# Optimization experiments

Hardware: AMD Instinct MI355X
Metric: run time of the kernel (lower is better)

The kernel has to match this reference:

```python
import jax, jax.numpy as jnp
import numpy as np

NEG_INF = -1e9  # matches torch masked_fill value


def setup_inputs() -> dict:
    key = jax.random.key(0)
    k1, k2, k3, k4, k5 = jax.random.split(key, 5)
    B, H, T, D = 2, 16, 2048, 64
    q = jax.random.normal(k1, (B, H, T, D), dtype=jnp.float32)
    k = jax.random.normal(k2, (B, H, T, D), dtype=jnp.float32)
    v = jax.random.normal(k3, (B, H, T, D), dtype=jnp.float32)
    mask = jax.random.randint(k4, (B, 1, 1, T), 0, 2, dtype=jnp.int32)
    relative_position_bias = jax.random.normal(k5, (1, H, T, T), dtype=jnp.float32)
    return {"q": q, "k": k, "v": v, "mask": mask,
            "relative_position_bias": relative_position_bias}


def reference(q, k, v, mask, relative_position_bias):
    head_dim = q.shape[-1]
    scale = 1.0 / jnp.sqrt(jnp.float32(head_dim)).astype(q.dtype)
    # scores: (B, H, T_q, T_k)
    scores = jnp.einsum('bhqd,bhkd->bhqk', q, k) * scale
    scores = scores + relative_position_bias
    scores = jnp.where(mask == 0, jnp.asarray(NEG_INF, scores.dtype), scores)
    attn = jax.nn.softmax(scores, axis=-1)
    # dropout p=0.0 -> identity
    output = jnp.einsum('bhqk,bhkd->bhqd', attn, v)
    return output, attn
```

## Files before the change

kernel.cpp:

```cpp
#include <hip/hip_runtime.h>

#define DEVI __device__ __forceinline__

typedef __attribute__((ext_vector_type(8))) short s16x8;
typedef __attribute__((ext_vector_type(4))) short s16x4;
typedef __attribute__((ext_vector_type(4))) float f32x4;

constexpr int B_ = 2, H_ = 16, T_ = 2048, D_ = 64;
constexpr int QT = 16;
constexpr int THREADS = 512;
constexpr int SROW = T_ + 8;
constexpr float SCALE = 0.125f;
constexpr float NEG_INF = -1e9f;

DEVI unsigned short f2bf(float x) {
    unsigned int u = __builtin_bit_cast(unsigned int, x);
    u = u + 0x7fffu + ((u >> 16) & 1u);
    return (unsigned short)(u >> 16);
}
DEVI float bf2f(unsigned short h) {
    unsigned int u = ((unsigned int)h) << 16;
    return __builtin_bit_cast(float, u);
}
DEVI unsigned short f2h(float x) {
    _Float16 h = (_Float16)x;
    return __builtin_bit_cast(unsigned short, h);
}
DEVI float h2f(unsigned short u) {
    _Float16 h = __builtin_bit_cast(_Float16, u);
    return (float)h;
}

DEVI void split8(const f32x4 a, const f32x4 b, s16x8& hi, s16x8& lo) {
#pragma unroll
    for (int e = 0; e < 4; ++e) {
        unsigned short u = f2bf(a[e]);
        hi[e] = (short)u; lo[e] = (short)f2bf(a[e] - bf2f(u));
        unsigned short v = f2bf(b[e]);
        hi[4 + e] = (short)v; lo[4 + e] = (short)f2bf(b[e] - bf2f(v));
    }
}

__global__ __launch_bounds__(THREADS, 4)
void attn_kernel(const float* __restrict__ qp, const float* __restrict__ kp,
                 const float* __restrict__ vp, const int* __restrict__ maskp,
                 const float* __restrict__ biasp, float* __restrict__ outp,
                 float* __restrict__ attnp)
{
    __shared__ alignas(16) unsigned short S[QT][SROW];
    __shared__ alignas(16) float ORED[8][QT][16];
    __shared__ float ML[QT][2];

    const int tid  = threadIdx.x;
    const int lane = tid & 63;
    const int w    = tid >> 6;
    const int r16  = lane & 15;
    const int g4   = lane >> 4;

    const int bid = blockIdx.x;
    const int qt  = bid & 127;
    const int b   = (bid >> 7) & 1;
    const int h   = bid >> 8;
    const int q0  = qt * QT;

    const size_t bh = (size_t)(b * H_ + h);
    const float* qb    = qp + (bh * T_ + q0) * D_;
    const float* kb    = kp + bh * T_ * D_;
    const float* vb    = vp + bh * T_ * D_;
    const float* biasb = biasp + (size_t)h * T_ * T_ + (size_t)q0 * T_;
    const int*   maskb = maskp + b * T_;
    float* outb  = outp  + (bh * T_ + q0) * D_;
    float* attnb = attnp + (bh * T_ + q0) * T_;

    s16x8 qh0, qh1, ql0, ql1;
    {
        const float* qrow = qb + (size_t)r16 * D_ + g4 * 8;
        const f32x4 a0 = *(const f32x4*)(qrow);
        const f32x4 a1 = *(const f32x4*)(qrow + 4);
        const f32x4 b0 = *(const f32x4*)(qrow + 32);
        const f32x4 b1 = *(const f32x4*)(qrow + 36);
        split8(a0, a1, qh0, ql0);
        split8(b0, b1, qh1, ql1);
    }

    for (int t = w; t < T_ / 16; t += 8) {
        const int c0 = t * 16;
        const float* krow = kb + (size_t)(c0 + r16) * D_ + g4 * 8;
        const f32x4 k0 = *(const f32x4*)(krow);
        const f32x4 k1 = *(const f32x4*)(krow + 4);
        const f32x4 k2 = *(const f32x4*)(krow + 32);
        const f32x4 k3 = *(const f32x4*)(krow + 36);
        s16x8 bh0, bl0, bh1, bl1;
        split8(k0, k1, bh0, bl0);
        split8(k2, k3, bh1, bl1);

        f32x4 acc = {0.f, 0.f, 0.f, 0.f};
        acc = __builtin_amdgcn_mfma_f32_16x16x32_bf16(qh0, bh0, acc, 0, 0, 0);
        acc = __builtin_amdgcn_mfma_f32_16x16x32_bf16(qh1, bh1, acc, 0, 0, 0);
        acc = __builtin_amdgcn_mfma_f32_16x16x32_bf16(ql0, bh0, acc, 0, 0, 0);
        acc = __builtin_amdgcn_mfma_f32_16x16x32_bf16(ql1, bh1, acc, 0, 0, 0);
        acc = __builtin_amdgcn_mfma_f32_16x16x32_bf16(qh0, bl0, acc, 0, 0, 0);
        acc = __builtin_amdgcn_mfma_f32_16x16x32_bf16(qh1, bl1, acc, 0, 0, 0);

        const int col = c0 + r16;
        const int mv  = maskb[col];
        const float* bp = biasb + (size_t)(g4 * 4) * T_ + col;
#pragma unroll
        for (int j = 0; j < 4; ++j) {
            float s = acc[j] * SCALE + bp[(size_t)j * T_];
            if (mv == 0) s = NEG_INF;
            S[g4 * 4 + j][col] = f2h(s);
        }
    }
    __syncthreads();

    {
        const int row = tid >> 5;
        const int c   = tid & 31;
        float m = -3.0e38f;
#pragma unroll
        for (int i = 0; i < 16; ++i) {
            s16x4 sv = *(const s16x4*)&S[row][c * 4 + i * 128];
            m = fmaxf(m, fmaxf(fmaxf(h2f((unsigned short)sv[0]), h2f((unsigned short)sv[1])),
                               fmaxf(h2f((unsigned short)sv[2]), h2f((unsigned short)sv[3]))));
        }
#pragma unroll
        for (int off = 16; off >= 1; off >>= 1) m = fmaxf(m, __shfl_xor(m, off));
        if (m < -1.0e30f) m = 0.f;
        float l = 0.f;
#pragma unroll
        for (int i = 0; i < 16; ++i) {
            s16x4 sv = *(const s16x4*)&S[row][c * 4 + i * 128];
            l += __expf(h2f((unsigned short)sv[0]) - m) + __expf(h2f((unsigned short)sv[1]) - m)
               + __expf(h2f((unsigned short)sv[2]) - m) + __expf(h2f((unsigned short)sv[3]) - m);
        }
#pragma unroll
        for (int off = 16; off >= 1; off >>= 1) l += __shfl_xor(l, off);
        if (c == 0) { ML[row][0] = m; ML[row][1] = (l > 0.f) ? 1.f / l : 0.f; }
    }
    __syncthreads();

    {
        const int row = tid >> 5;
        const int c   = tid & 31;
        const float m    = ML[row][0];
        const float invl = ML[row][1];
        float* arow = attnb + (size_t)row * T_;
#pragma unroll 4
        for (int i = 0; i < 16; ++i) {
            const int col = c * 4 + i * 128;
            s16x4 sv = *(const s16x4*)&S[row][col];
            float p0 = __expf(h2f((unsigned short)sv[0]) - m) * invl;
            float p1 = __expf(h2f((unsigned short)sv[1]) - m) * invl;
            float p2 = __expf(h2f((unsigned short)sv[2]) - m) * invl;
            float p3 = __expf(h2f((unsigned short)sv[3]) - m) * invl;
            f32x4 pv = {p0, p1, p2, p3};
            __builtin_nontemporal_store(pv, (f32x4*)(arow + col));
            s16x4 pb;
            pb[0] = (short)f2bf(p0); pb[1] = (short)f2bf(p1);
            pb[2] = (short)f2bf(p2); pb[3] = (short)f2bf(p3);
            *(s16x4*)&S[row][col] = pb;
        }
    }
    __syncthreads();

    {
        const int dt = w & 3;
        const int ks = w >> 2;
        const int d0 = dt * 16 + r16;
        f32x4 acc = {0.f, 0.f, 0.f, 0.f};
        const float* vcol = vb + d0;
#pragma unroll 2
        for (int step = 0; step < 32; ++step) {
            const int kloc = ks * 1024 + step * 32 + g4 * 8;
            s16x8 pa = *(const s16x8*)&S[r16][kloc];
            const float* vptr = vcol + (size_t)kloc * D_;
            s16x8 vf;
#pragma unroll
            for (int e = 0; e < 8; ++e) vf[e] = (short)f2bf(vptr[(size_t)e * D_]);
            acc = __builtin_amdgcn_mfma_f32_16x16x32_bf16(pa, vf, acc, 0, 0, 0);
        }
#pragma unroll
        for (int j = 0; j < 4; ++j) ORED[w][g4 * 4 + j][r16] = acc[j];
    }
    __syncthreads();

    if (tid < 256) {
        const int row = tid >> 4;
        const int dc  = (tid & 15) * 4;
        const int dt  = dc >> 4;
        f32x4 o;
#pragma unroll
        for (int e = 0; e < 4; ++e)
            o[e] = ORED[dt][row][(dc & 15) + e] + ORED[dt + 4][row][(dc & 15) + e];
        *(f32x4*)(outb + (size_t)row * D_ + dc) = o;
    }
}

extern "C" void kernel_launch(void* const* d_in, const int* in_sizes, int n_in,
                              void* d_out, int out_size, void* d_ws, size_t ws_size,
                              hipStream_t stream) {
    const float* q    = (const float*)d_in[0];
    const float* k    = (const float*)d_in[1];
    const float* v    = (const float*)d_in[2];
    const int*   mask = (const int*)d_in[3];
    const float* bias = (const float*)d_in[4];
    float* out  = (float*)d_out;
    float* attn = out + (size_t)B_ * H_ * T_ * D_;

    dim3 grid(B_ * H_ * (T_ / QT));
    attn_kernel<<<grid, THREADS, 0, stream>>>(q, k, v, mask, bias, out, attn);
}
```

Measured before the change: 1.049 ms.

## Pre-split K and pre-transpose V to bf16 in workspace, drop softmax max pass

Two helper kernels run first. One splits K into bf16 hi/lo arrays, and the other converts V to bf16 in transposed layout, both stored in the workspace. The attention kernel then loads contiguous bf16 fragments instead of converting fp32 K per tile and gathering V with strided scalar loads. Softmax now stores exp(s) directly as bf16 without subtracting the row max, which removes a full max pass, and the 1/l normalization is folded into the output write. The risks are overflow for large scores and lower precision in the attn output, since probabilities pass through bf16. The new path depends on the workspace being large enough, and otherwise falls back to the old kernel.

```diff
diff --git a/kernel.cpp b/kernel.cpp
--- a/kernel.cpp
+++ b/kernel.cpp
@@ -12,6 +12,8 @@
 constexpr int SROW = T_ + 8;
 constexpr float SCALE = 0.125f;
 constexpr float NEG_INF = -1e9f;
+constexpr size_t NKV = (size_t)B_ * H_ * T_ * D_;
+constexpr size_t WS_REQ = 3 * NKV * sizeof(unsigned short);
 
 DEVI unsigned short f2bf(float x) {
     unsigned int u = __builtin_bit_cast(unsigned int, x);
@@ -41,11 +43,199 @@
     }
 }
 
+__global__ __launch_bounds__(256)
+void ksplit_kernel(const float* __restrict__ kp, unsigned short* __restrict__ khi,
+                   unsigned short* __restrict__ klo)
+{
+    const size_t i = ((size_t)blockIdx.x * 256 + threadIdx.x) * 8;
+    const f32x4 a = *(const f32x4*)(kp + i);
+    const f32x4 b = *(const f32x4*)(kp + i + 4);
+    s16x8 hi, lo;
+    split8(a, b, hi, lo);
+    *(s16x8*)(khi + i) = hi;
+    *(s16x8*)(klo + i) = lo;
+}
+
+__global__ __launch_bounds__(256)
+void vtrans_kernel(const float* __restrict__ vp, unsigned short* __restrict__ vt)
+{
+    __shared__ unsigned short tile[64][68];
+    const int bh = blockIdx.x >> 5;
+    const int kt = blockIdx.x & 31;
+    const int k0 = kt * 64;
+    const int tid = threadIdx.x;
+    const float* vsrc = vp + ((size_t)bh * T_ + k0) * D_;
+#pragma unroll
+    for (int it = 0; it < 4; ++it) {
+        const int idx = it * 256 + tid;
+        const int row = idx >> 4;
+        const int c4  = (idx & 15) * 4;
+        const f32x4 w = *(const f32x4*)(vsrc + (size_t)row * D_ + c4);
+        s16x4 p;
+#pragma unroll
+        for (int e = 0; e < 4; ++e) p[e] = (short)f2bf(w[e]);
+        *(s16x4*)&tile[row][c4] = p;
+    }
+    __syncthreads();
+#pragma unroll
+    for (int it = 0; it < 2; ++it) {
+        const int idx = it * 256 + tid;
+        const int d  = idx >> 3;
+        const int k8 = (idx & 7) * 8;
+        s16x8 o;
+#pragma unroll
+        for (int j = 0; j < 8; ++j) o[j] = (short)tile[k8 + j][d];
+        *(s16x8*)(vt + ((size_t)bh * D_ + d) * T_ + k0 + k8) = o;
+    }
+}
+
 __global__ __launch_bounds__(THREADS, 4)
-void attn_kernel(const float* __restrict__ qp, const float* __restrict__ kp,
-                 const float* __restrict__ vp, const int* __restrict__ maskp,
-                 const float* __restrict__ biasp, float* __restrict__ outp,
-                 float* __restrict__ attnp)
+void attn_kernel_v2(const float* __restrict__ qp,
+                    const unsigned short* __restrict__ khi,
+                    const unsigned short* __restrict__ klo,
+                    const unsigned short* __restrict__ vt,
+                    const int* __restrict__ maskp,
+                    const float* __restrict__ biasp, float* __restrict__ outp,
+                    float* __restrict__ attnp)
+{
+    __shared__ alignas(16) unsigned short S[QT][SROW];
+    __shared__ alignas(16) float ORED[8][QT][16];
+    __shared__ float ML[QT];
+
+    const int tid  = threadIdx.x;
+    const int lane = tid & 63;
+    const int w    = tid >> 6;
+    const int r16  = lane & 15;
+    const int g4   = lane >> 4;
+
+    const int bid = blockIdx.x;
+    const int qt  = bid & 127;
+    const int b   = (bid >> 7) & 1;
+    const int h   = bid >> 8;
+    const int q0  = qt * QT;
+
+    const size_t bh = (size_t)(b * H_ + h);
+    const float* qb    = qp + (bh * T_ + q0) * D_;
+    const unsigned short* khb = khi + bh * T_ * D_;
+    const unsigned short* klb = klo + bh * T_ * D_;
+    const unsigned short* vtb = vt  + bh * T_ * D_;
+    const float* biasb = biasp + (size_t)h * T_ * T_ + (size_t)q0 * T_;
+    const int*   maskb = maskp + b * T_;
+    float* outb  = outp  + (bh * T_ + q0) * D_;
+    float* attnb = attnp + (bh * T_ + q0) * T_;
+
+    s16x8 qh0, qh1, ql0, ql1;
+    {
+        const float* qrow = qb + (size_t)r16 * D_ + g4 * 8;
+        const f32x4 a0 = *(const f32x4*)(qrow);
+        const f32x4 a1 = *(const f32x4*)(qrow + 4);
+        const f32x4 b0 = *(const f32x4*)(qrow + 32);
+        const f32x4 b1 = *(const f32x4*)(qrow + 36);
+        split8(a0, a1, qh0, ql0);
+        split8(b0, b1, qh1, ql1);
+    }
+
+    for (int t = w; t < T_ / 16; t += 8) {
+        const int c0  = t * 16;
+        const int col = c0 + r16;
+        const size_t fro = (size_t)col * D_ + g4 * 8;
+        const s16x8 bh0 = *(const s16x8*)(khb + fro);
+        const s16x8 bh1 = *(const s16x8*)(khb + fro + 32);
+        const s16x8 bl0 = *(const s16x8*)(klb + fro);
+        const s16x8 bl1 = *(const s16x8*)(klb + fro + 32);
+
+        f32x4 acc = {0.f, 0.f, 0.f, 0.f};
+        acc = __builtin_amdgcn_mfma_f32_16x16x32_bf16(qh0, bh0, acc, 0, 0, 0);
+        acc = __builtin_amdgcn_mfma_f32_16x16x32_bf16(qh1, bh1, acc, 0, 0, 0);
+        acc = __builtin_amdgcn_mfma_f32_16x16x32_bf16(ql0, bh0, acc, 0, 0, 0);
+        acc = __builtin_amdgcn_mfma_f32_16x16x32_bf16(ql1, bh1, acc, 0, 0, 0);
+        acc = __builtin_amdgcn_mfma_f32_16x16x32_bf16(qh0, bl0, acc, 0, 0, 0);
+        acc = __builtin_amdgcn_mfma_f32_16x16x32_bf16(qh1, bl1, acc, 0, 0, 0);
+
+        const int mv = maskb[col];
+        const float* bp = biasb + (size_t)(g4 * 4) * T_ + col;
+#pragma unroll
+        for (int j = 0; j < 4; ++j) {
+            float s = acc[j] * SCALE + bp[(size_t)j * T_];
+            if (mv == 0) s = NEG_INF;
+            S[g4 * 4 + j][col] = f2bf(__expf(s));
+        }
+    }
+    __syncthreads();
+
+    {
+        const int row = tid >> 5;
+        const int c   = tid & 31;
+        float l = 0.f;
+#pragma unroll
+        for (int i = 0; i < 8; ++i) {
+            s16x8 sv = *(const s16x8*)&S[row][c * 8 + i * 256];
+#pragma unroll
+            for (int e = 0; e < 8; ++e) l += bf2f((unsigned short)sv[e]);
+        }
+#pragma unroll
+        for (int off = 16; off >= 1; off >>= 1) l += __shfl_xor(l, off);
+        if (c == 0) ML[row] = (l > 0.f) ? 1.f / l : 0.f;
+    }
+    __syncthreads();
+
+    {
+        const int row = tid >> 5;
+        const int c   = tid & 31;
+        const float invl = ML[row];
+        float* arow = attnb + (size_t)row * T_;
+#pragma unroll 4
+        for (int i = 0; i < 8; ++i) {
+            const int col = c * 8 + i * 256;
+            s16x8 sv = *(const s16x8*)&S[row][col];
+            f32x4 p0, p1;
+#pragma unroll
+            for (int e = 0; e < 4; ++e) {
+                p0[e] = bf2f((unsigned short)sv[e]) * invl;
+                p1[e] = bf2f((unsigned short)sv[4 + e]) * invl;
+            }
+            __builtin_nontemporal_store(p0, (f32x4*)(arow + col));
+            __builtin_nontemporal_store(p1, (f32x4*)(arow + col + 4));
+        }
+    }
+    __syncthreads();
+
+    {
+        const int dt = w & 3;
+        const int ks = w >> 2;
+        const int d0 = dt * 16 + r16;
+        f32x4 acc = {0.f, 0.f, 0.f, 0.f};
+        const unsigned short* vrow = vtb + (size_t)d0 * T_;
+#pragma unroll 4
+        for (int step = 0; step < 32; ++step) {
+            const int kloc = ks * 1024 + step * 32 + g4 * 8;
+            s16x8 pa = *(const s16x8*)&S[r16][kloc];
+            s16x8 vf = *(const s16x8*)(vrow + kloc);
+            acc = __builtin_amdgcn_mfma_f32_16x16x32_bf16(pa, vf, acc, 0, 0, 0);
+        }
+#pragma unroll
+        for (int j = 0; j < 4; ++j) ORED[w][g4 * 4 + j][r16] = acc[j];
+    }
+    __syncthreads();
+
+    if (tid < 256) {
+        const int row = tid >> 4;
+        const int dc  = (tid & 15) * 4;
+        const int dt  = dc >> 4;
+        const float invl = ML[row];
+        f32x4 o;
+#pragma unroll
+        for (int e = 0; e < 4; ++e)
+            o[e] = (ORED[dt][row][(dc & 15) + e] + ORED[dt + 4][row][(dc & 15) + e]) * invl;
+        *(f32x4*)(outb + (size_t)row * D_ + dc) = o;
+    }
+}
+
+__global__ __launch_bounds__(THREADS, 4)
+void attn_kernel_fb(const float* __restrict__ qp, const float* __restrict__ kp,
+                    const float* __restrict__ vp, const int* __restrict__ maskp,
+                    const float* __restrict__ biasp, float* __restrict__ outp,
+                    float* __restrict__ attnp)
 {
     __shared__ alignas(16) unsigned short S[QT][SROW];
     __shared__ alignas(16) float ORED[8][QT][16];
@@ -209,5 +399,15 @@
     float* attn = out + (size_t)B_ * H_ * T_ * D_;
 
     dim3 grid(B_ * H_ * (T_ / QT));
-    attn_kernel<<<grid, THREADS, 0, stream>>>(q, k, v, mask, bias, out, attn);
-}
+
+    if (ws_size >= WS_REQ) {
+        unsigned short* khi = (unsigned short*)d_ws;
+        unsigned short* klo = khi + NKV;
+        unsigned short* vt  = klo + NKV;
+        ksplit_kernel<<<dim3((unsigned)(NKV / 8 / 256)), 256, 0, stream>>>(k, khi, klo);
+        vtrans_kernel<<<dim3(B_ * H_ * (T_ / 64)), 256, 0, stream>>>(v, vt);
+        attn_kernel_v2<<<grid, THREADS, 0, stream>>>(q, khi, klo, vt, mask, bias, out, attn);
+    } else {
+        attn_kernel_fb<<<grid, THREADS, 0, stream>>>(q, k, v, mask, bias, out, attn);
+    }
+}
```

Measured after the change: 1.052 ms. No clear change (+0.3%).
